# Kernel tuning notes

Measured on AMD Instinct MI355X. Metric: run time of the kernel, lower is better.

Reference implementation:

```python
import jax, jax.numpy as jnp
import numpy as np

N_NODES = 100000
N_EDGES = 600000
N_CLASS = 26
HIDDEN = 128


def setup_inputs() -> dict:
    key = jax.random.key(0)
    ks = jax.random.split(key, 8)
    x = jax.random.normal(ks[0], (N_NODES, N_CLASS), dtype=jnp.float32)
    edge_index = jax.random.randint(ks[1], (2, N_EDGES), 0, N_NODES, dtype=jnp.int64)
    edge_weight = jax.random.uniform(ks[2], (N_EDGES,), dtype=jnp.float32)
    W1 = jax.random.normal(ks[3], (N_CLASS, HIDDEN), dtype=jnp.float32) * (1.0 / np.sqrt(N_CLASS))
    b1 = jnp.zeros((HIDDEN,), dtype=jnp.float32)
    W2 = jax.random.normal(ks[4], (HIDDEN, HIDDEN), dtype=jnp.float32) * (1.0 / np.sqrt(HIDDEN))
    b2 = jnp.zeros((HIDDEN,), dtype=jnp.float32)
    Wfc = jax.random.normal(ks[5], (HIDDEN, N_CLASS), dtype=jnp.float32) * (1.0 / np.sqrt(HIDDEN))
    bfc = jnp.zeros((N_CLASS,), dtype=jnp.float32)
    return {"x": x, "edge_index": edge_index, "edge_weight": edge_weight,
            "W1": W1, "b1": b1, "W2": W2, "b2": b2, "Wfc": Wfc, "bfc": bfc}


def _gcn_norm(edge_index, edge_weight, n_nodes):
    # PyG gcn_norm: add self-loops (weight 1), symmetric deg^-1/2 normalization.
    loop = jnp.arange(n_nodes, dtype=edge_index.dtype)
    row = jnp.concatenate([edge_index[0], loop])  # source
    col = jnp.concatenate([edge_index[1], loop])  # destination
    w = jnp.concatenate([edge_weight, jnp.ones((n_nodes,), edge_weight.dtype)])
    deg = jax.ops.segment_sum(w, col, num_segments=n_nodes)
    d_inv_sqrt = jnp.where(deg > 0, jax.lax.rsqrt(jnp.maximum(deg, 1e-12)), 0.0)
    norm = d_inv_sqrt[row] * w * d_inv_sqrt[col]
    return row, col, norm


def _gcn_conv(x, row, col, norm, W, b, n_nodes):
    h = x @ W                              # [N, out]
    msg = norm[:, None] * h[row]           # gather + scale, [E+N, out]
    out = jax.ops.segment_sum(msg, col, num_segments=n_nodes)  # scatter-add
    return out + b


def reference(x, edge_index, edge_weight, W1, b1, W2, b2, Wfc, bfc):
    n = x.shape[0]
    row, col, norm = _gcn_norm(edge_index, edge_weight, n)
    h = jax.nn.relu(_gcn_conv(x, row, col, norm, W1, b1, n))
    h = jax.nn.relu(_gcn_conv(h, row, col, norm, W2, b2, n))
    return h @ Wfc + bfc
```

## Files before the change

kernel.cpp:

```cpp
#include <hip/hip_runtime.h>

#define NNODES 100000
#define NEDGES 600000
#define NCLASS 26
#define HID    128

#define SHIFT  9
#define BCOLS  512
#define NBKT   196
#define EPB    1024
#define NBE    586
#define NH     (NBKT * NBE)

typedef __attribute__((ext_vector_type(8))) _Float16 f16x8;
typedef __attribute__((ext_vector_type(4))) float f32x4;

__device__ inline unsigned short f2h(float f) {
    union { _Float16 h; unsigned short s; } c;
    c.h = (_Float16)f;
    return c.s;
}
__device__ inline unsigned int packh(float a, float b) {
    return (unsigned int)f2h(a) | ((unsigned int)f2h(b) << 16);
}
__device__ inline float hlo(unsigned int p) {
    union { unsigned short s; _Float16 h; } c;
    c.s = (unsigned short)p;
    return (float)c.h;
}
__device__ inline float hhi(unsigned int p) {
    union { unsigned short s; _Float16 h; } c;
    c.s = (unsigned short)(p >> 16);
    return (float)c.h;
}

__device__ inline void fma16_u8(float* acc, float v, uint4 g) {
    unsigned int u[4] = { g.x, g.y, g.z, g.w };
#pragma unroll
    for (int w = 0; w < 4; w++) {
        acc[w * 4 + 0] = fmaf(v, (float)( u[w]        & 0xffu), acc[w * 4 + 0]);
        acc[w * 4 + 1] = fmaf(v, (float)((u[w] >> 8 ) & 0xffu), acc[w * 4 + 1]);
        acc[w * 4 + 2] = fmaf(v, (float)((u[w] >> 16) & 0xffu), acc[w * 4 + 2]);
        acc[w * 4 + 3] = fmaf(v, (float)( u[w] >> 24        ), acc[w * 4 + 3]);
    }
}

__global__ __launch_bounds__(256) void histA_k(const int* __restrict__ col,
                                               int* __restrict__ H) {
    __shared__ int h[NBKT];
    int t = threadIdx.x;
    for (int i = t; i < NBKT; i += 256) h[i] = 0;
    __syncthreads();
    int base = blockIdx.x * EPB;
#pragma unroll
    for (int u = 0; u < 4; u++) {
        int e = base + t + u * 256;
        if (e < NEDGES) atomicAdd(&h[col[e] >> SHIFT], 1);
    }
    __syncthreads();
    for (int i = t; i < NBKT; i += 256) H[i * NBE + blockIdx.x] = h[i];
}

__global__ void scanH1_k(const int* __restrict__ in, int* __restrict__ incl,
                         int* __restrict__ aux, int n) {
    __shared__ int s[256];
    int t = threadIdx.x, gi = blockIdx.x * 256 + t;
    s[t] = (gi < n) ? in[gi] : 0;
    __syncthreads();
    for (int off = 1; off < 256; off <<= 1) {
        int x = (t >= off) ? s[t - off] : 0;
        __syncthreads();
        s[t] += x;
        __syncthreads();
    }
    if (gi < n) incl[gi] = s[t];
    if (t == 255) aux[blockIdx.x] = s[255];
}

__global__ void scan2_k(int* __restrict__ aux, int n) {
    __shared__ int s[512];
    int t = threadIdx.x;
    s[t] = (t < n) ? aux[t] : 0;
    __syncthreads();
    for (int off = 1; off < 512; off <<= 1) {
        int x = (t >= off) ? s[t - off] : 0;
        __syncthreads();
        s[t] += x;
        __syncthreads();
    }
    if (t < n) aux[t] = s[t];
}

__device__ inline int exoff(const int* __restrict__ incl, const int* __restrict__ H,
                            const int* __restrict__ aux, int gi) {
    int add = (gi >= 256) ? aux[(gi >> 8) - 1] : 0;
    return incl[gi] - H[gi] + add;
}

__global__ __launch_bounds__(256) void partB_k(const int* __restrict__ row,
                                               const int* __restrict__ col,
                                               const float* __restrict__ w,
                                               const int* __restrict__ incl,
                                               const int* __restrict__ H,
                                               const int* __restrict__ aux,
                                               uint2* __restrict__ rw,
                                               unsigned short* __restrict__ lc) {
    __shared__ int off[NBKT];
    __shared__ int cur[NBKT];
    int t = threadIdx.x;
    for (int i = t; i < NBKT; i += 256) {
        off[i] = exoff(incl, H, aux, i * NBE + blockIdx.x);
        cur[i] = 0;
    }
    __syncthreads();
    int base = blockIdx.x * EPB;
#pragma unroll
    for (int u = 0; u < 4; u++) {
        int e = base + t + u * 256;
        if (e < NEDGES) {
            int c = col[e], b = c >> SHIFT;
            int p = off[b] + atomicAdd(&cur[b], 1);
            rw[p] = make_uint2((unsigned int)row[e], __float_as_uint(w[e]));
            lc[p] = (unsigned short)(c & (BCOLS - 1));
        }
    }
}

__global__ __launch_bounds__(256) void segbp_k(const uint2* __restrict__ rw,
                                               const unsigned short* __restrict__ lc,
                                               const int* __restrict__ incl,
                                               const int* __restrict__ H,
                                               const int* __restrict__ aux,
                                               int* __restrict__ rowptr,
                                               float* __restrict__ dis,
                                               uint2* __restrict__ meta) {
    __shared__ int   cnt[BCOLS];
    __shared__ float ws[BCOLS];
    __shared__ int   rpl[BCOLS];
    __shared__ int   ps[256];
    int b = blockIdx.x, t = threadIdx.x;
    int c0 = b << SHIFT;
    int ncols = min(BCOLS, NNODES - c0);
    for (int i = t; i < BCOLS; i += 256) { cnt[i] = 0; ws[i] = 0.f; }
    __syncthreads();
    int s    = exoff(incl, H, aux, b * NBE);
    int eend = (b == NBKT - 1) ? NEDGES : exoff(incl, H, aux, (b + 1) * NBE);
    for (int e = s + t; e < eend; e += 256) {
        uint2 m = rw[e];
        int l = lc[e];
        atomicAdd(&cnt[l], 1);
        atomicAdd(&ws[l], __uint_as_float(m.y));
    }
    __syncthreads();
    for (int i = t; i < ncols; i += 256) dis[c0 + i] = rsqrtf(1.0f + ws[i]);
    int a0 = cnt[2 * t], a1 = cnt[2 * t + 1];
    ps[t] = a0 + a1;
    __syncthreads();
    for (int off = 1; off < 256; off <<= 1) {
        int x = (t >= off) ? ps[t - off] : 0;
        __syncthreads();
        ps[t] += x;
        __syncthreads();
    }
    int ex = (t > 0) ? ps[t - 1] : 0;
    rpl[2 * t]     = s + ex;
    rpl[2 * t + 1] = s + ex + a0;
    if (2 * t     < ncols) rowptr[c0 + 2 * t]     = s + ex;
    if (2 * t + 1 < ncols) rowptr[c0 + 2 * t + 1] = s + ex + a0;
    if (b == NBKT - 1 && t == 0) rowptr[NNODES] = NEDGES;
    cnt[2 * t] = 0; cnt[2 * t + 1] = 0;
    __syncthreads();
    for (int e = s + t; e < eend; e += 256) {
        uint2 m = rw[e];
        int l = lc[e];
        int pos = rpl[l] + atomicAdd(&cnt[l], 1);
        meta[pos] = make_uint2(m.x, m.y);
    }
}

__global__ __launch_bounds__(256) void prep_k(const float* __restrict__ W2,
                                              const float* __restrict__ W1,
                                              const float* __restrict__ Wfc,
                                              const float* __restrict__ x,
                                              const float* __restrict__ dis,
                                              unsigned short* __restrict__ wt,
                                              unsigned short* __restrict__ w1t,
                                              unsigned short* __restrict__ wfct,
                                              unsigned int* __restrict__ xq,
                                              float* __restrict__ xscale) {
    int b = blockIdx.x, t = threadIdx.x;
    if (b < 64) {
        int idx = b * 256 + t;
        int c = idx >> 7, k = idx & 127;
        wt[c * 128 + k] = f2h(W2[k * 128 + c]);
    } else if (b < 80) {
        int idx = (b - 64) * 256 + t;
        int c = idx >> 5, k = idx & 31;
        w1t[c * 32 + k] = (k < NCLASS) ? f2h(W1[k * 128 + c]) : (unsigned short)0;
    } else if (b < 96) {
        int idx = (b - 80) * 256 + t;
        int c = idx >> 7, k = idx & 127;
        wfct[c * 128 + k] = (c < NCLASS) ? f2h(Wfc[k * NCLASS + c]) : (unsigned short)0;
    } else {
        int idx = (b - 96) * 256 + t;
        int r = idx >> 3, l = idx & 7;
        if (r < NNODES) {
            float d = dis[r];
            float v[4]; float m = 0.f;
#pragma unroll
            for (int k = 0; k < 4; k++) {
                int f = l * 4 + k;
                v[k] = (f < NCLASS) ? d * x[r * NCLASS + f] : 0.f;
                m = fmaxf(m, fabsf(v[k]));
            }
#pragma unroll
            for (int s = 1; s < 8; s <<= 1)
                m = fmaxf(m, __shfl_xor(m, s));
            float inv = (m > 0.f) ? 127.f / m : 0.f;
            unsigned int q = 0;
#pragma unroll
            for (int k = 0; k < 4; k++) {
                int qq = (int)rintf(v[k] * inv) + 128;
                q |= ((unsigned int)qq & 0xffu) << (8 * k);
            }
            xq[(size_t)r * 8 + l] = q;
            if (l == 0) xscale[r] = m * (1.f / 127.f);
        }
    }
}

__global__ __launch_bounds__(256) void agg26_k(const int* __restrict__ rowptr,
                                               const uint2* __restrict__ meta,
                                               const unsigned int* __restrict__ xq,
                                               const float* __restrict__ xscale,
                                               const float* __restrict__ dis,
                                               unsigned int* __restrict__ aggx) {
    int node = blockIdx.x * 32 + (threadIdx.x >> 3);
    int l8 = threadIdx.x & 7;

    float vs = xscale[node];
    float vsum = vs;
    unsigned int s = xq[(size_t)node * 8 + l8];
    float acc[4];
    acc[0] = vs * (float)( s        & 0xffu);
    acc[1] = vs * (float)((s >> 8 ) & 0xffu);
    acc[2] = vs * (float)((s >> 16) & 0xffu);
    acc[3] = vs * (float)( s >> 24        );
    int j = rowptr[node], jend = rowptr[node + 1];
    for (; j < jend; j++) {
        uint2 m = meta[j];
        float v = __uint_as_float(m.y) * xscale[m.x];
        unsigned int g = xq[(size_t)m.x * 8 + l8];
        vsum += v;
        acc[0] = fmaf(v, (float)( g        & 0xffu), acc[0]);
        acc[1] = fmaf(v, (float)((g >> 8 ) & 0xffu), acc[1]);
        acc[2] = fmaf(v, (float)((g >> 16) & 0xffu), acc[2]);
        acc[3] = fmaf(v, (float)( g >> 24        ), acc[3]);
    }
    float b128 = 128.f * vsum;
    float d = dis[node];
    ((uint2*)aggx)[(size_t)node * 8 + l8] =
        make_uint2(packh(d * (acc[0] - b128), d * (acc[1] - b128)),
                   packh(d * (acc[2] - b128), d * (acc[3] - b128)));
}

__global__ __launch_bounds__(256) void gemm12_k(const unsigned short* __restrict__ aggx,
                                                const unsigned short* __restrict__ w1t,
                                                const float* __restrict__ b1,
                                                const unsigned short* __restrict__ wt,
                                                const float* __restrict__ dis,
                                                unsigned char* __restrict__ C8,
                                                float* __restrict__ hscale, int N) {
    __shared__ unsigned short h1s[64 * 136];
    __shared__ unsigned short Ws[128 * 72];
    const int tid  = threadIdx.x;
    const int wv = tid >> 6, lane = tid & 63;
    const int quad = lane >> 4, l16 = lane & 15;
    const int row0 = blockIdx.x * 64;
    const int wrow = wv * 16;

#pragma unroll
    for (int jj = 0; jj < 4; jj++) {
        int idx = tid + jj * 256;
        int r = idx >> 3, ku = idx & 7;
        *(uint4*)&Ws[r * 72 + ku * 8] = *(const uint4*)&wt[(size_t)r * 128 + ku * 8];
    }

    {
        int ar = row0 + wrow + l16;
        f16x8 af1 = (ar < N) ? *(const f16x8*)&aggx[(size_t)ar * 32 + quad * 8]
                             : (f16x8)(_Float16)0.f;
#pragma unroll
        for (int n = 0; n < 8; n++) {
            f16x8 bw = *(const f16x8*)&w1t[(n * 16 + l16) * 32 + quad * 8];
            f32x4 hacc = __builtin_amdgcn_mfma_f32_16x16x32_f16(af1, bw, (f32x4)0.f, 0, 0, 0);
            int col = n * 16 + l16;
            float bv = b1[col];
#pragma unroll
            for (int r = 0; r < 4; r++)
                h1s[(wrow + quad * 4 + r) * 136 + col] = f2h(fmaxf(hacc[r] + bv, 0.f));
        }
    }
    __syncthreads();

    f16x8 af[4];
#pragma unroll
    for (int kc = 0; kc < 4; kc++)
        af[kc] = *(const f16x8*)&h1s[(wrow + l16) * 136 + kc * 32 + quad * 8];

    f32x4 acc[8];
#pragma unroll
    for (int n = 0; n < 8; n++) acc[n] = (f32x4)0.f;

    for (int c = 0; c < 2; c++) {
        if (c == 1) {
            __syncthreads();
#pragma unroll
            for (int jj = 0; jj < 4; jj++) {
                int idx = tid + jj * 256;
                int r = idx >> 3, ku = idx & 7;
                *(uint4*)&Ws[r * 72 + ku * 8] =
                    *(const uint4*)&wt[(size_t)r * 128 + 64 + ku * 8];
            }
            __syncthreads();
        }
#pragma unroll
        for (int n = 0; n < 8; n++) {
#pragma unroll
            for (int kc = 0; kc < 2; kc++) {
                f16x8 bfr = *(const f16x8*)&Ws[(n * 16 + l16) * 72 + kc * 32 + quad * 8];
                acc[n] = __builtin_amdgcn_mfma_f32_16x16x32_f16(
                    af[c * 2 + kc], bfr, acc[n], 0, 0, 0);
            }
        }
    }

    const int rbase = row0 + wrow + quad * 4;
    float dv[4];
#pragma unroll
    for (int r = 0; r < 4; r++)
        dv[r] = (rbase + r < N) ? dis[rbase + r] : 0.f;

    float vv[8][4];
    float rmax[4] = { 0.f, 0.f, 0.f, 0.f };
#pragma unroll
    for (int n = 0; n < 8; n++)
#pragma unroll
        for (int r = 0; r < 4; r++) {
            vv[n][r] = dv[r] * acc[n][r];
            rmax[r] = fmaxf(rmax[r], fabsf(vv[n][r]));
        }
#pragma unroll
    for (int s = 1; s < 16; s <<= 1) {
#pragma unroll
        for (int r = 0; r < 4; r++)
            rmax[r] = fmaxf(rmax[r], __shfl_xor(rmax[r], s));
    }
    float inv[4];
#pragma unroll
    for (int r = 0; r < 4; r++)
        inv[r] = (rmax[r] > 0.f) ? 127.f / rmax[r] : 0.f;
    if (l16 == 0) {
#pragma unroll
        for (int r = 0; r < 4; r++)
            if (rbase + r < N) hscale[rbase + r] = rmax[r] * (1.f / 127.f);
    }
#pragma unroll
    for (int n = 0; n < 8; n++) {
        int col = n * 16 + l16;
#pragma unroll
        for (int r = 0; r < 4; r++) {
            if (rbase + r < N) {
                int q = (int)rintf(vv[n][r] * inv[r]);
                C8[(size_t)(rbase + r) * 128 + col] = (unsigned char)(q + 128);
            }
        }
    }
}

__global__ __launch_bounds__(256) void aggfc_k(const int* __restrict__ rowptr,
                                               const uint2* __restrict__ meta,
                                               const uint4* __restrict__ h8,
                                               const float* __restrict__ hscale,
                                               const float* __restrict__ dis,
                                               const float* __restrict__ b2,
                                               const unsigned short* __restrict__ wfct,
                                               const float* __restrict__ bfc,
                                               float* __restrict__ out, int N) {
    __shared__ unsigned short h2s[64 * 136];
    const int tid = threadIdx.x;
    const int wv = tid >> 6, lane = tid & 63;
    const int grp = lane >> 3, l8 = lane & 7;
    const int nbase = blockIdx.x * 64;

    for (int p = 0; p < 2; p++) {
        int r = wv * 16 + p * 8 + grp;
        int node = nbase + r;
        float acc[16];
#pragma unroll
        for (int k = 0; k < 16; k++) acc[k] = 0.f;
        float d = 0.f;
        if (node < N) {
            d = dis[node];
            float vs = hscale[node];
            float vsum = vs;
            uint4 s0 = h8[(size_t)node * 8 + l8];
            fma16_u8(acc, vs, s0);
            int j = rowptr[node], jend = rowptr[node + 1];
            for (; j < jend; j++) {
                uint2 m = meta[j];
                float v = __uint_as_float(m.y) * hscale[m.x];
                uint4 g = h8[(size_t)m.x * 8 + l8];
                vsum += v;
                fma16_u8(acc, v, g);
            }
            float b128 = 128.f * vsum;
#pragma unroll
            for (int k = 0; k < 16; k++) acc[k] -= b128;
        }
        unsigned int wpk[8];
#pragma unroll
        for (int q = 0; q < 4; q++) {
            float4 bv = ((const float4*)b2)[l8 * 4 + q];
            float a0 = fmaxf(fmaf(d, acc[q * 4 + 0], bv.x), 0.f);
            float a1 = fmaxf(fmaf(d, acc[q * 4 + 1], bv.y), 0.f);
            float a2 = fmaxf(fmaf(d, acc[q * 4 + 2], bv.z), 0.f);
            float a3 = fmaxf(fmaf(d, acc[q * 4 + 3], bv.w), 0.f);
            if (node >= N) { a0 = a1 = a2 = a3 = 0.f; }
            wpk[q * 2]     = packh(a0, a1);
            wpk[q * 2 + 1] = packh(a2, a3);
        }
        *(uint4*)&h2s[r * 136 + l8 * 16] =
            make_uint4(wpk[0], wpk[1], wpk[2], wpk[3]);
        *(uint4*)&h2s[r * 136 + l8 * 16 + 8] =
            make_uint4(wpk[4], wpk[5], wpk[6], wpk[7]);
    }

    const int q = lane >> 4, m = lane & 15;
    f16x8 af[4];
#pragma unroll
    for (int ks = 0; ks < 4; ks++)
        af[ks] = *(const f16x8*)&h2s[(wv * 16 + m) * 136 + ks * 32 + q * 8];

#pragma unroll
    for (int n = 0; n < 2; n++) {
        f32x4 o = (f32x4)0.f;
#pragma unroll
        for (int ks = 0; ks < 4; ks++) {
            f16x8 bfr = *(const f16x8*)&wfct[(size_t)(n * 16 + m) * 128 + ks * 32 + q * 8];
            o = __builtin_amdgcn_mfma_f32_16x16x32_f16(af[ks], bfr, o, 0, 0, 0);
        }
        int col = n * 16 + m;
        if (col < NCLASS) {
            float bv = bfc[col];
            int r0 = nbase + wv * 16 + q * 4;
#pragma unroll
            for (int r = 0; r < 4; r++) {
                if (r0 + r < N)
                    out[(size_t)(r0 + r) * NCLASS + col] = o[r] + bv;
            }
        }
    }
}

extern "C" void kernel_launch(void* const* d_in, const int* in_sizes, int n_in,
                              void* d_out, int out_size, void* d_ws, size_t ws_size,
                              hipStream_t stream) {
    const float* x   = (const float*)d_in[0];
    const int*   ei  = (const int*)d_in[1];
    const float* ew  = (const float*)d_in[2];
    const float* W1  = (const float*)d_in[3];
    const float* b1  = (const float*)d_in[4];
    const float* W2  = (const float*)d_in[5];
    const float* b2  = (const float*)d_in[6];
    const float* Wfc = (const float*)d_in[7];
    const float* bfc = (const float*)d_in[8];
    float* out = (float*)d_out;

    const int N = NNODES;
    const int* erow = ei;
    const int* ecol = ei + NEDGES;

    float* fws    = (float*)d_ws;
    float* dis    = fws;
    int*   rowptr = (int*)(fws + 100000);
    int*   H      = (int*)(fws + 200004);
    int*   incl   = (int*)(fws + 314860);
    int*   aux    = (int*)(fws + 429716);
    uint2* rw     = (uint2*)(fws + 430228);
    unsigned short* lc = (unsigned short*)(fws + 1630228);
    uint2* meta   = (uint2*)(fws + 1930228);
    unsigned short* wt16   = (unsigned short*)(fws + 3130228);
    unsigned short* w1t16  = (unsigned short*)(fws + 3138420);
    unsigned short* wfct16 = (unsigned short*)(fws + 3140468);
    unsigned int*   xq     = (unsigned int*)(fws + 3142516);
    float*          xscale = (float*)(fws + 3942516);
    unsigned int*   aggx   = (unsigned int*)(fws + 4742516);
    unsigned char*  hB8    = (unsigned char*)(fws + 6342516);
    float*          hscale = (float*)(fws + 9542516);

    const int gScan = (NH + 255) / 256;
    const int gA26  = N / 32;
    const int gPrep = 96 + (N * 8 + 255) / 256;
    const int g64   = (N + 63) / 64;

    histA_k<<<NBE, 256, 0, stream>>>(ecol, H);
    scanH1_k<<<gScan, 256, 0, stream>>>(H, incl, aux, NH);
    scan2_k<<<1, 512, 0, stream>>>(aux, gScan);
    partB_k<<<NBE, 256, 0, stream>>>(erow, ecol, ew, incl, H, aux, rw, lc);
    segbp_k<<<NBKT, 256, 0, stream>>>(rw, lc, incl, H, aux, rowptr, dis, meta);

    prep_k<<<gPrep, 256, 0, stream>>>(W2, W1, Wfc, x, dis, wt16, w1t16, wfct16,
                                      xq, xscale);

    agg26_k<<<gA26, 256, 0, stream>>>(rowptr, meta, xq, xscale, dis, aggx);
    gemm12_k<<<g64, 256, 0, stream>>>((const unsigned short*)aggx, w1t16, b1,
                                      wt16, dis, hB8, hscale, N);

    aggfc_k<<<g64, 256, 0, stream>>>(rowptr, meta, (const uint4*)hB8, hscale, dis, b2,
                                     wfct16, bfc, out, N);
}
```

Before: 184.9 us.

## Fuse first-layer aggregation into the two-layer GEMM kernel

Removes the separate agg26 kernel and performs the int8 neighbor aggregation of x directly inside the GEMM kernel. Each lane now gathers 8 features per edge instead of 4, so a node uses 4 lanes instead of 8. The aggregated row goes straight into the MFMA A-fragment in registers, avoiding the fp16 aggx round trip through global memory and one kernel launch. The cost is fewer threads per node, so the gather has less parallelism and more latency per node, and the GEMM waves stall on the irregular edge loop.

```diff
diff --git a/kernel.cpp b/kernel.cpp
--- a/kernel.cpp
+++ b/kernel.cpp
@@ -229,48 +229,16 @@
     }
 }
 
-__global__ __launch_bounds__(256) void agg26_k(const int* __restrict__ rowptr,
-                                               const uint2* __restrict__ meta,
-                                               const unsigned int* __restrict__ xq,
-                                               const float* __restrict__ xscale,
-                                               const float* __restrict__ dis,
-                                               unsigned int* __restrict__ aggx) {
-    int node = blockIdx.x * 32 + (threadIdx.x >> 3);
-    int l8 = threadIdx.x & 7;
-
-    float vs = xscale[node];
-    float vsum = vs;
-    unsigned int s = xq[(size_t)node * 8 + l8];
-    float acc[4];
-    acc[0] = vs * (float)( s        & 0xffu);
-    acc[1] = vs * (float)((s >> 8 ) & 0xffu);
-    acc[2] = vs * (float)((s >> 16) & 0xffu);
-    acc[3] = vs * (float)( s >> 24        );
-    int j = rowptr[node], jend = rowptr[node + 1];
-    for (; j < jend; j++) {
-        uint2 m = meta[j];
-        float v = __uint_as_float(m.y) * xscale[m.x];
-        unsigned int g = xq[(size_t)m.x * 8 + l8];
-        vsum += v;
-        acc[0] = fmaf(v, (float)( g        & 0xffu), acc[0]);
-        acc[1] = fmaf(v, (float)((g >> 8 ) & 0xffu), acc[1]);
-        acc[2] = fmaf(v, (float)((g >> 16) & 0xffu), acc[2]);
-        acc[3] = fmaf(v, (float)( g >> 24        ), acc[3]);
-    }
-    float b128 = 128.f * vsum;
-    float d = dis[node];
-    ((uint2*)aggx)[(size_t)node * 8 + l8] =
-        make_uint2(packh(d * (acc[0] - b128), d * (acc[1] - b128)),
-                   packh(d * (acc[2] - b128), d * (acc[3] - b128)));
-}
-
-__global__ __launch_bounds__(256) void gemm12_k(const unsigned short* __restrict__ aggx,
-                                                const unsigned short* __restrict__ w1t,
-                                                const float* __restrict__ b1,
-                                                const unsigned short* __restrict__ wt,
-                                                const float* __restrict__ dis,
-                                                unsigned char* __restrict__ C8,
-                                                float* __restrict__ hscale, int N) {
+__global__ __launch_bounds__(256) void agggemm_k(const int* __restrict__ rowptr,
+                                                 const uint2* __restrict__ meta,
+                                                 const uint2* __restrict__ xq2,
+                                                 const float* __restrict__ xscale,
+                                                 const unsigned short* __restrict__ w1t,
+                                                 const float* __restrict__ b1,
+                                                 const unsigned short* __restrict__ wt,
+                                                 const float* __restrict__ dis,
+                                                 unsigned char* __restrict__ C8,
+                                                 float* __restrict__ hscale, int N) {
     __shared__ unsigned short h1s[64 * 136];
     __shared__ unsigned short Ws[128 * 72];
     const int tid  = threadIdx.x;
@@ -286,20 +254,54 @@
         *(uint4*)&Ws[r * 72 + ku * 8] = *(const uint4*)&wt[(size_t)r * 128 + ku * 8];
     }
 
+    f16x8 af1 = (f16x8)(_Float16)0.f;
     {
         int ar = row0 + wrow + l16;
-        f16x8 af1 = (ar < N) ? *(const f16x8*)&aggx[(size_t)ar * 32 + quad * 8]
-                             : (f16x8)(_Float16)0.f;
-#pragma unroll
-        for (int n = 0; n < 8; n++) {
-            f16x8 bw = *(const f16x8*)&w1t[(n * 16 + l16) * 32 + quad * 8];
-            f32x4 hacc = __builtin_amdgcn_mfma_f32_16x16x32_f16(af1, bw, (f32x4)0.f, 0, 0, 0);
-            int col = n * 16 + l16;
-            float bv = b1[col];
-#pragma unroll
-            for (int r = 0; r < 4; r++)
-                h1s[(wrow + quad * 4 + r) * 136 + col] = f2h(fmaxf(hacc[r] + bv, 0.f));
-        }
+        if (ar < N) {
+            float vs = xscale[ar];
+            float vsum = vs;
+            uint2 s = xq2[(size_t)ar * 4 + quad];
+            float acc[8];
+            acc[0] = vs * (float)( s.x        & 0xffu);
+            acc[1] = vs * (float)((s.x >> 8 ) & 0xffu);
+            acc[2] = vs * (float)((s.x >> 16) & 0xffu);
+            acc[3] = vs * (float)( s.x >> 24        );
+            acc[4] = vs * (float)( s.y        & 0xffu);
+            acc[5] = vs * (float)((s.y >> 8 ) & 0xffu);
+            acc[6] = vs * (float)((s.y >> 16) & 0xffu);
+            acc[7] = vs * (float)( s.y >> 24        );
+            int j = rowptr[ar], jend = rowptr[ar + 1];
+            for (; j < jend; j++) {
+                uint2 m = meta[j];
+                float v = __uint_as_float(m.y) * xscale[m.x];
+                uint2 g = xq2[(size_t)m.x * 4 + quad];
+                vsum += v;
+                acc[0] = fmaf(v, (float)( g.x        & 0xffu), acc[0]);
+                acc[1] = fmaf(v, (float)((g.x >> 8 ) & 0xffu), acc[1]);
+                acc[2] = fmaf(v, (float)((g.x >> 16) & 0xffu), acc[2]);
+                acc[3] = fmaf(v, (float)( g.x >> 24        ), acc[3]);
+                acc[4] = fmaf(v, (float)( g.y        & 0xffu), acc[4]);
+                acc[5] = fmaf(v, (float)((g.y >> 8 ) & 0xffu), acc[5]);
+                acc[6] = fmaf(v, (float)((g.y >> 16) & 0xffu), acc[6]);
+                acc[7] = fmaf(v, (float)( g.y >> 24        ), acc[7]);
+            }
+            float b128 = 128.f * vsum;
+            float d = dis[ar];
+#pragma unroll
+            for (int k = 0; k < 8; k++)
+                af1[k] = (_Float16)(d * (acc[k] - b128));
+        }
+    }
+
+#pragma unroll
+    for (int n = 0; n < 8; n++) {
+        f16x8 bw = *(const f16x8*)&w1t[(n * 16 + l16) * 32 + quad * 8];
+        f32x4 hacc = __builtin_amdgcn_mfma_f32_16x16x32_f16(af1, bw, (f32x4)0.f, 0, 0, 0);
+        int col = n * 16 + l16;
+        float bv = b1[col];
+#pragma unroll
+        for (int r = 0; r < 4; r++)
+            h1s[(wrow + quad * 4 + r) * 136 + col] = f2h(fmaxf(hacc[r] + bv, 0.f));
     }
     __syncthreads();
 
@@ -308,9 +310,9 @@
     for (int kc = 0; kc < 4; kc++)
         af[kc] = *(const f16x8*)&h1s[(wrow + l16) * 136 + kc * 32 + quad * 8];
 
-    f32x4 acc[8];
-#pragma unroll
-    for (int n = 0; n < 8; n++) acc[n] = (f32x4)0.f;
+    f32x4 acc2[8];
+#pragma unroll
+    for (int n = 0; n < 8; n++) acc2[n] = (f32x4)0.f;
 
     for (int c = 0; c < 2; c++) {
         if (c == 1) {
@@ -329,8 +331,8 @@
 #pragma unroll
             for (int kc = 0; kc < 2; kc++) {
                 f16x8 bfr = *(const f16x8*)&Ws[(n * 16 + l16) * 72 + kc * 32 + quad * 8];
-                acc[n] = __builtin_amdgcn_mfma_f32_16x16x32_f16(
-                    af[c * 2 + kc], bfr, acc[n], 0, 0, 0);
+                acc2[n] = __builtin_amdgcn_mfma_f32_16x16x32_f16(
+                    af[c * 2 + kc], bfr, acc2[n], 0, 0, 0);
             }
         }
     }
@@ -347,7 +349,7 @@
     for (int n = 0; n < 8; n++)
 #pragma unroll
         for (int r = 0; r < 4; r++) {
-            vv[n][r] = dv[r] * acc[n][r];
+            vv[n][r] = dv[r] * acc2[n][r];
             rmax[r] = fmaxf(rmax[r], fabsf(vv[n][r]));
         }
 #pragma unroll
@@ -495,12 +497,10 @@
     unsigned short* wfct16 = (unsigned short*)(fws + 3140468);
     unsigned int*   xq     = (unsigned int*)(fws + 3142516);
     float*          xscale = (float*)(fws + 3942516);
-    unsigned int*   aggx   = (unsigned int*)(fws + 4742516);
     unsigned char*  hB8    = (unsigned char*)(fws + 6342516);
     float*          hscale = (float*)(fws + 9542516);
 
     const int gScan = (NH + 255) / 256;
-    const int gA26  = N / 32;
     const int gPrep = 96 + (N * 8 + 255) / 256;
     const int g64   = (N + 63) / 64;
 
@@ -513,9 +513,8 @@
     prep_k<<<gPrep, 256, 0, stream>>>(W2, W1, Wfc, x, dis, wt16, w1t16, wfct16,
                                       xq, xscale);
 
-    agg26_k<<<gA26, 256, 0, stream>>>(rowptr, meta, xq, xscale, dis, aggx);
-    gemm12_k<<<g64, 256, 0, stream>>>((const unsigned short*)aggx, w1t16, b1,
-                                      wt16, dis, hB8, hscale, N);
+    agggemm_k<<<g64, 256, 0, stream>>>(rowptr, meta, (const uint2*)xq, xscale,
+                                       w1t16, b1, wt16, dis, hB8, hscale, N);
 
     aggfc_k<<<g64, 256, 0, stream>>>(rowptr, meta, (const uint4*)hB8, hscale, dis, b2,
                                      wfct16, bfc, out, N);
```

After: 182.1 us. No clear change (-1.5%).
